# Kernel tuning notes

Hardware: AMD Instinct MI355X
Metric: run time of the kernel (lower is better)

## Reference

```python
import jax, jax.numpy as jnp
import numpy as np
from jax import lax

B, L = 16, 2048
D_TOK, D_TIS = 256, 64
D_MODEL = D_TOK + D_TIS          # 320
EXPAND = 2
D_INNER = EXPAND * D_MODEL       # 640
D_STATE = 16
D_CONV = 4
DT_RANK = (D_MODEL + 15) // 16   # 20 (ceil(d_model/16), Mamba default)
H_OUT = 128
VOCAB = 65                       # len(CODON_MAP_DNA)+1
N_TISSUES = 30
MAX_NORM = 2.0


def _embed_maxnorm(W, idx):
    # torch nn.Embedding(max_norm=2): looked-up rows are renormalized to norm<=2
    e = W[idx]
    n = jnp.linalg.norm(e, axis=-1, keepdims=True)
    return e * jnp.minimum(1.0, MAX_NORM / jnp.maximum(n, 1e-12))


def setup_inputs() -> dict:
    key = jax.random.key(0)
    ks = jax.random.split(key, 18)
    s = 0.02
    seq_W = jax.random.normal(ks[3], (VOCAB, D_TOK), dtype=jnp.float32)
    seq_W = seq_W.at[0].set(0.0)  # padding_idx=0
    A_log = jnp.log(jnp.broadcast_to(jnp.arange(1, D_STATE + 1, dtype=jnp.float32), (D_INNER, D_STATE)))
    return {
        "rna_data_pad": jax.random.randint(ks[0], (B, L), 0, VOCAB).astype(jnp.int32),
        "tissue_id": jax.random.randint(ks[1], (B,), 0, N_TISSUES).astype(jnp.int32),
        "seq_lengths": jax.random.randint(ks[2], (B,), 1, L + 1).astype(jnp.int32),
        "seq_W": seq_W,
        "tissue_W": jax.random.normal(ks[4], (N_TISSUES, D_TIS), dtype=jnp.float32),
        "in_proj_W": jax.random.normal(ks[5], (2 * D_INNER, D_MODEL), dtype=jnp.float32) * s,
        "conv_w": jax.random.normal(ks[6], (D_INNER, 1, D_CONV), dtype=jnp.float32) * s,
        "conv_b": jnp.zeros((D_INNER,), dtype=jnp.float32),
        "x_proj_W": jax.random.normal(ks[7], (DT_RANK + 2 * D_STATE, D_INNER), dtype=jnp.float32) * s,
        "dt_proj_W": jax.random.normal(ks[8], (D_INNER, DT_RANK), dtype=jnp.float32) * s,
        "dt_proj_b": jax.random.uniform(ks[9], (D_INNER,), minval=-4.0, maxval=-2.0),
        "A_log": A_log,
        "D_skip": jnp.ones((D_INNER,), dtype=jnp.float32),
        "out_proj_W": jax.random.normal(ks[10], (D_MODEL, D_INNER), dtype=jnp.float32) * s,
        "p1_W": jax.random.normal(ks[11], (H_OUT, D_MODEL), dtype=jnp.float32) * s,
        "p1_b": jnp.zeros((H_OUT,), dtype=jnp.float32),
        "p2_W": jax.random.normal(ks[12], (1, H_OUT), dtype=jnp.float32) * s,
        "p2_b": jnp.zeros((1,), dtype=jnp.float32),
    }


def reference(rna_data_pad, tissue_id, seq_lengths, seq_W, tissue_W, in_proj_W,
              conv_w, conv_b, x_proj_W, dt_proj_W, dt_proj_b, A_log, D_skip,
              out_proj_W, p1_W, p1_b, p2_W, p2_b):
    b, l = rna_data_pad.shape
    # embeddings + tissue broadcast + mask
    seq_emb = _embed_maxnorm(seq_W, rna_data_pad)            # [B,L,D_TOK]
    tis_emb = _embed_maxnorm(tissue_W, tissue_id)            # [B,D_TIS]
    tis_exp = jnp.broadcast_to(tis_emb[:, None, :], (b, l, tis_emb.shape[-1]))
    x = jnp.concatenate([seq_emb, tis_exp], axis=-1)          # [B,L,D_MODEL]
    x = x * (rna_data_pad != 0)[..., None]
    # Mamba block
    xz = x @ in_proj_W.T                                      # [B,L,2*D_INNER]
    xm, z = jnp.split(xz, 2, axis=-1)
    xt = xm.transpose(0, 2, 1)                                # [B,D_INNER,L]
    conv = lax.conv_general_dilated(
        xt, conv_w, window_strides=(1,), padding=[(D_CONV - 1, 0)],
        feature_group_count=D_INNER,
        dimension_numbers=("NCH", "OIH", "NCH")) + conv_b[None, :, None]
    xm = jax.nn.silu(conv).transpose(0, 2, 1)                 # [B,L,D_INNER]
    x_dbl = xm @ x_proj_W.T                                   # [B,L,DT_RANK+2*D_STATE]
    dt, Bm, Cm = jnp.split(x_dbl, [DT_RANK, DT_RANK + D_STATE], axis=-1)
    delta = jax.nn.softplus(dt @ dt_proj_W.T + dt_proj_b)     # [B,L,D_INNER]
    A = -jnp.exp(A_log)                                       # [D_INNER,D_STATE]
    # selective scan over time
    xs = (delta.transpose(1, 0, 2), Bm.transpose(1, 0, 2),
          Cm.transpose(1, 0, 2), xm.transpose(1, 0, 2))
    h0 = jnp.zeros((b, D_INNER, D_STATE), dtype=xm.dtype)

    def step(h, t):
        dl, bt, ct, ut = t                                    # [B,di],[B,ds],[B,ds],[B,di]
        dA = jnp.exp(dl[:, :, None] * A)                      # [B,di,ds]
        dBu = (dl * ut)[:, :, None] * bt[:, None, :]          # [B,di,ds]
        h = dA * h + dBu
        y = jnp.einsum("bds,bs->bd", h, ct)
        return h, y

    _, ys = lax.scan(step, h0, xs)                            # ys: [L,B,D_INNER]
    y = ys.transpose(1, 0, 2) + xm * D_skip
    y = y * jax.nn.silu(z)
    out = y @ out_proj_W.T                                    # [B,L,D_MODEL]
    # gather last valid timestep
    out_last = out[jnp.arange(b), seq_lengths - 1]            # [B,D_MODEL]
    h1 = jax.nn.relu(out_last @ p1_W.T + p1_b)
    return h1 @ p2_W.T + p2_b                                 # [B,1]
```

## Files before the change

### kernel.cpp

```cpp
#include <hip/hip_runtime.h>
#include <hip/hip_bf16.h>
#include <math.h>

#define B_      16
#define L_      2048
#define D_MODEL 320
#define D_INNER 640
#define D_STATE 16
#define DT_RANK 20
#define H_OUT   128
#define VOCAB   65
#define N_TIS   30
#define TT      8
#define ST      64
#define NCHUNK  16
#define CHLEN   (L_/NCHUNK)

static constexpr size_t OFF_MSEQ  = 0;
static constexpr size_t OFF_MTIS  = OFF_MSEQ + VOCAB*1280;
static constexpr size_t OFF_YSCAN = OFF_MTIS + N_TIS*1280;
static constexpr size_t OFF_CLAST = OFF_YSCAN + B_*D_INNER;
static constexpr size_t OFF_XD20  = OFF_CLAST + B_*16;
static constexpr size_t OFF_BBAR  = OFF_XD20 + (size_t)B_*L_*20;
static constexpr size_t OFF_PC    = OFF_BBAR + (size_t)B_*D_STATE*L_;
static constexpr size_t OFF_SC    = OFF_PC + (size_t)B_*NCHUNK*40*256;

__device__ __forceinline__ float silu_f(float x) { return x / (1.0f + __expf(-x)); }

__global__ __launch_bounds__(256) void k_mbuild(
    const float* __restrict__ seqW, const float* __restrict__ tisW,
    const float* __restrict__ inW, float* __restrict__ ws)
{
    __shared__ float a_l[256];
    __shared__ float red[4];
    int v = blockIdx.x, tid = threadIdx.x;
    int K, wofs; const float* src; float* dstM;
    if (v < VOCAB) { K = 256; wofs = 0;   src = seqW + (size_t)v*256;        dstM = ws + OFF_MSEQ + (size_t)v*1280; }
    else           { K = 64;  wofs = 256; src = tisW + (size_t)(v-VOCAB)*64; dstM = ws + OFF_MTIS + (size_t)(v-VOCAB)*1280; }
    float x = (tid < K) ? src[tid] : 0.0f;
    float ss = x * x;
    #pragma unroll
    for (int o = 32; o; o >>= 1) ss += __shfl_xor(ss, o);
    if ((tid & 63) == 0) red[tid >> 6] = ss;
    __syncthreads();
    float tot = red[0] + red[1] + red[2] + red[3];
    float scale = fminf(1.0f, 2.0f / fmaxf(sqrtf(tot), 1e-12f));
    if (tid < K) a_l[tid] = x * scale;
    __syncthreads();

    int j = blockIdx.y * 256 + tid;
    const float* w = inW + (size_t)j*320 + wofs;
    float ac0 = 0.f, ac1 = 0.f, ac2 = 0.f, ac3 = 0.f;
    #pragma unroll 4
    for (int k = 0; k < K; k += 4) {
        float4 w4 = *(const float4*)(w + k);
        ac0 += a_l[k+0]*w4.x; ac1 += a_l[k+1]*w4.y;
        ac2 += a_l[k+2]*w4.z; ac3 += a_l[k+3]*w4.w;
    }
    dstM[j] = (ac0 + ac1) + (ac2 + ac3);
}

__global__ __launch_bounds__(256) void k_xdbl(
    const int* __restrict__ idx, const int* __restrict__ tissue_id,
    const int* __restrict__ seq_lengths,
    const float* __restrict__ conv_w, const float* __restrict__ conv_b,
    const float* __restrict__ xW, float* __restrict__ ws)
{
    __shared__ float u_l[TT*641];
    __shared__ float xd_l[TT*36];
    __shared__ int   idx_l[TT+3];
    int b = blockIdx.y;
    int t0 = blockIdx.x * TT;
    int t_last = seq_lengths[b] - 1;
    if (t0 > t_last) return;
    int tid = threadIdx.x;
    const float* Mseq = ws + OFF_MSEQ;
    const float* Mtis = ws + OFF_MTIS;
    int tis = tissue_id[b];
    if (tid < TT+3) {
        int t = t0 - 3 + tid;
        idx_l[tid] = (t >= 0) ? idx[b*L_ + t] : 0;
    }
    __syncthreads();

    for (int d = tid; d < D_INNER; d += 256) {
        float w0 = conv_w[d*4+0], w1 = conv_w[d*4+1], w2 = conv_w[d*4+2], w3 = conv_w[d*4+3];
        float cb = conv_b[d];
        float mt = Mtis[(size_t)tis*1280 + d];
        float xzv[TT+3];
        #pragma unroll
        for (int k = 0; k < TT+3; ++k) {
            int row = idx_l[k];
            xzv[k] = row ? (Mseq[(size_t)row*1280 + d] + mt) : 0.0f;
        }
        #pragma unroll
        for (int t = 0; t < TT; ++t) {
            float c = cb;
            c = fmaf(w0, xzv[t+0], c);
            c = fmaf(w1, xzv[t+1], c);
            c = fmaf(w2, xzv[t+2], c);
            c = fmaf(w3, xzv[t+3], c);
            u_l[t*641 + d] = silu_f(c);
        }
    }
    __syncthreads();

    {
        int w = tid >> 6, l = tid & 63;
        float wreg[9][10];
        #pragma unroll
        for (int kk = 0; kk < 9; ++kk) {
            const float* xr = xW + (size_t)(w + 4*kk)*D_INNER + l;
            #pragma unroll
            for (int i = 0; i < 10; ++i) wreg[kk][i] = xr[64*i];
        }
        for (int t = 0; t < TT; ++t) {
            float p[9];
            #pragma unroll
            for (int kk = 0; kk < 9; ++kk) p[kk] = 0.f;
            #pragma unroll
            for (int i = 0; i < 10; ++i) {
                float ui = u_l[t*641 + l + 64*i];
                #pragma unroll
                for (int kk = 0; kk < 9; ++kk) p[kk] = fmaf(wreg[kk][i], ui, p[kk]);
            }
            #pragma unroll
            for (int o = 32; o; o >>= 1) {
                #pragma unroll
                for (int kk = 0; kk < 9; ++kk) p[kk] += __shfl_xor(p[kk], o);
            }
            if (l == t) {
                #pragma unroll
                for (int kk = 0; kk < 9; ++kk) xd_l[t*36 + w + 4*kk] = p[kk];
            }
        }
        if (t_last < t0 + TT) {
            int tl = t_last - t0;
            float pc[4];
            #pragma unroll
            for (int k = 0; k < 4; ++k) pc[k] = 0.f;
            #pragma unroll
            for (int i = 0; i < 10; ++i) {
                float ui = u_l[tl*641 + l + 64*i];
                #pragma unroll
                for (int k = 0; k < 4; ++k)
                    pc[k] = fmaf(xW[(size_t)(36 + w + 4*k)*D_INNER + l + 64*i], ui, pc[k]);
            }
            #pragma unroll
            for (int o = 32; o; o >>= 1) {
                #pragma unroll
                for (int k = 0; k < 4; ++k) pc[k] += __shfl_xor(pc[k], o);
            }
            if (l == 0) {
                #pragma unroll
                for (int k = 0; k < 4; ++k) ws[OFF_CLAST + b*16 + w + 4*k] = pc[k];
            }
        }
    }
    __syncthreads();

    {
        int nt = min(TT, t_last - t0 + 1);
        int cnt = nt * 20;
        float* dst = ws + OFF_XD20 + ((size_t)b*L_ + t0)*20;
        for (int o = tid; o < cnt; o += 256) {
            int t = o / 20, r = o - t*20;
            dst[o] = xd_l[t*36 + r];
        }
        int cntB = nt * 16;
        if (tid < cntB) {
            int s, tt;
            if (nt == TT) { s = tid >> 3; tt = tid & 7; }
            else          { s = tid / nt; tt = tid - s*nt; }
            ws[OFF_BBAR + ((size_t)b*D_STATE + s)*L_ + t0 + tt] = xd_l[tt*36 + 20 + s];
        }
    }
}

__global__ __launch_bounds__(256) void k_scanc(
    const int* __restrict__ idx, const int* __restrict__ tissue_id,
    const int* __restrict__ seq_lengths,
    const float* __restrict__ conv_w, const float* __restrict__ conv_b,
    const float* __restrict__ dtW, const float* __restrict__ dtb,
    const float* __restrict__ A_log, float* __restrict__ ws)
{
    __shared__ float xd_t[ST*20];
    __shared__ float dl_t[16*68];
    __shared__ float du_t[16*68];
    __shared__ float Bb_t[16*68];
    __shared__ float sdred[16*17];
    __shared__ int   idx_t[ST+3];

    int b = blockIdx.y, dg = blockIdx.x, c = blockIdx.z;
    int t_last = seq_lengths[b] - 1;
    int t_begin = c * CHLEN;
    if (t_begin > t_last) return;
    int t_end = min(t_begin + CHLEN - 1, t_last);
    int tid = threadIdx.x;
    int dl = tid >> 4, s = tid & 15;
    int dd = tid & 15, tg = tid >> 4;
    int d_own = dg*16 + dd;
    int tis = tissue_id[b];
    const float* Mseq = ws + OFF_MSEQ;

    float dtw_r[20];
    #pragma unroll
    for (int i = 0; i < 20; i += 4) {
        float4 w4 = *(const float4*)(dtW + d_own*20 + i);
        dtw_r[i] = w4.x; dtw_r[i+1] = w4.y; dtw_r[i+2] = w4.z; dtw_r[i+3] = w4.w;
    }
    float4 cw4 = *(const float4*)(conv_w + d_own*4);
    float  cb  = conv_b[d_own];
    float  dtb_v = dtb[d_own];
    float  mt  = ws[OFF_MTIS + (size_t)tis*1280 + d_own];
    float As = -__expf(A_log[(dg*16 + dl)*D_STATE + s]) * 1.44269504089f;

    float h = 0.0f;
    float sdp = 0.0f;
    for (int t0 = t_begin; t0 <= t_end; t0 += ST) {
        int nt = min(ST, t_end - t0 + 1);
        if (tid < ST+3) {
            int t = t0 - 3 + tid;
            idx_t[tid] = (t >= 0 && t < L_) ? idx[b*L_ + t] : 0;
        }
        {
            const float4* src = (const float4*)(ws + OFF_XD20 + ((size_t)b*L_ + t0)*20);
            float4* dst = (float4*)xd_t;
            int cnt4 = nt * 5;
            for (int o = tid; o < cnt4; o += 256) dst[o] = src[o];
        }
        {
            int lr = tid >> 4, c4 = (tid & 15) * 4;
            if (c4 < nt)
                *(float4*)(Bb_t + lr*68 + c4) =
                    *(const float4*)(ws + OFF_BBAR + ((size_t)b*D_STATE + lr)*L_ + t0 + c4);
        }
        __syncthreads();

        {
            int ttb = tg * 4;
            if (ttb < nt) {
                float xz[7];
                #pragma unroll
                for (int k = 0; k < 7; ++k) {
                    int row = idx_t[ttb + k];
                    xz[k] = row ? (Mseq[(size_t)row*1280 + d_own] + mt) : 0.0f;
                }
                float dl4[4], du4[4];
                bool full = (ttb + 3 < nt);
                #pragma unroll
                for (int j = 0; j < 4; ++j) {
                    int tt = ttb + j;
                    if (full || tt < nt) {
                        float cc = cb;
                        cc = fmaf(cw4.x, xz[j+0], cc);
                        cc = fmaf(cw4.y, xz[j+1], cc);
                        cc = fmaf(cw4.z, xz[j+2], cc);
                        cc = fmaf(cw4.w, xz[j+3], cc);
                        float u = silu_f(cc);
                        const float* xr = xd_t + tt*20;
                        float x = dtb_v;
                        #pragma unroll
                        for (int r = 0; r < 20; r += 4) {
                            float4 x4 = *(const float4*)(xr + r);
                            x = fmaf(x4.x, dtw_r[r+0], x);
                            x = fmaf(x4.y, dtw_r[r+1], x);
                            x = fmaf(x4.z, dtw_r[r+2], x);
                            x = fmaf(x4.w, dtw_r[r+3], x);
                        }
                        float e = __expf(-fabsf(x));
                        float sp = fmaxf(x, 0.0f) + __logf(1.0f + e);
                        dl4[j] = sp;
                        du4[j] = sp * u;
                        sdp += sp;
                    } else { dl4[j] = 0.f; du4[j] = 0.f; }
                }
                if (full) {
                    *(float4*)(dl_t + dd*68 + ttb) = make_float4(dl4[0], dl4[1], dl4[2], dl4[3]);
                    *(float4*)(du_t + dd*68 + ttb) = make_float4(du4[0], du4[1], du4[2], du4[3]);
                } else {
                    for (int j = 0; j < 4 && ttb + j < nt; ++j) {
                        dl_t[dd*68 + ttb + j] = dl4[j];
                        du_t[dd*68 + ttb + j] = du4[j];
                    }
                }
            }
        }
        __syncthreads();

        {
            int q4 = nt >> 2;
            #pragma unroll 8
            for (int q = 0; q < q4; ++q) {
                float4 d4 = *(const float4*)(dl_t + dl*68 + 4*q);
                float4 u4 = *(const float4*)(du_t + dl*68 + 4*q);
                float4 b4 = *(const float4*)(Bb_t + s*68 + 4*q);
                h = fmaf(exp2f(d4.x*As), h, u4.x*b4.x);
                h = fmaf(exp2f(d4.y*As), h, u4.y*b4.y);
                h = fmaf(exp2f(d4.z*As), h, u4.z*b4.z);
                h = fmaf(exp2f(d4.w*As), h, u4.w*b4.w);
            }
            for (int tt = q4*4; tt < nt; ++tt) {
                float dlt = dl_t[dl*68 + tt];
                h = fmaf(exp2f(dlt * As), h, du_t[dl*68 + tt] * Bb_t[s*68 + tt]);
            }
        }
        __syncthreads();
    }
    sdred[tg*17 + dd] = sdp;
    __syncthreads();
    float sd = 0.0f;
    #pragma unroll
    for (int g = 0; g < 16; ++g) sd += sdred[g*17 + dl];
    float P = exp2f(As * sd);
    size_t base = (((size_t)b*NCHUNK + c)*40 + dg)*256 + tid;
    ws[OFF_PC + base] = P;
    ws[OFF_SC + base] = h;
}

__global__ __launch_bounds__(256) void k_comb(const int* __restrict__ seq_lengths,
                                              float* __restrict__ ws)
{
    int b = blockIdx.y, dg = blockIdx.x;
    int tid = threadIdx.x;
    int dl = tid >> 4, s = tid & 15;
    int t_last = seq_lengths[b] - 1;
    int ncv = t_last / CHLEN + 1;
    float h = 0.0f;
    for (int c = 0; c < ncv; ++c) {
        size_t base = (((size_t)b*NCHUNK + c)*40 + dg)*256 + tid;
        h = fmaf(ws[OFF_PC + base], h, ws[OFF_SC + base]);
    }
    float v = h * ws[OFF_CLAST + b*16 + s];
    v += __shfl_xor(v, 1); v += __shfl_xor(v, 2);
    v += __shfl_xor(v, 4); v += __shfl_xor(v, 8);
    if (s == 0) ws[OFF_YSCAN + (size_t)b*D_INNER + dg*16 + dl] = v;
}

__global__ __launch_bounds__(320) void k_final(
    const int* __restrict__ idx, const int* __restrict__ tissue_id,
    const int* __restrict__ seq_lengths,
    const float* __restrict__ conv_w, const float* __restrict__ conv_b,
    const float* __restrict__ Dskip, const float* __restrict__ outW,
    const float* __restrict__ p1W, const float* __restrict__ p1b,
    const float* __restrict__ p2W, const float* __restrict__ p2b,
    const float* __restrict__ ws, float* __restrict__ out)
{
    __shared__ float y_l[D_INNER];
    __shared__ float o_l[D_MODEL];
    __shared__ float h1_l[H_OUT];
    int b = blockIdx.x, tid = threadIdx.x;
    int t_last = seq_lengths[b] - 1;
    int tis = tissue_id[b];
    const float* Mseq = ws + OFF_MSEQ;
    const float* Mtis = ws + OFF_MTIS;
    int rows[4];
    #pragma unroll
    for (int k = 0; k < 4; ++k) {
        int t = t_last - 3 + k;
        rows[k] = (t >= 0) ? idx[b*L_ + t] : 0;
    }
    for (int d = tid; d < D_INNER; d += 320) {
        float conv = conv_b[d];
        const float* cw = conv_w + d*4;
        #pragma unroll
        for (int k = 0; k < 4; ++k) {
            int row = rows[k];
            float xzv = row ? (Mseq[(size_t)row*1280 + d] + Mtis[(size_t)tis*1280 + d]) : 0.0f;
            conv += cw[k] * xzv;
        }
        float u = silu_f(conv);
        int rowL = rows[3];
        float z = rowL ? (Mseq[(size_t)rowL*1280 + 640 + d] + Mtis[(size_t)tis*1280 + 640 + d]) : 0.0f;
        float ys = ws[OFF_YSCAN + (size_t)b*D_INNER + d];
        y_l[d] = (ys + u * Dskip[d]) * silu_f(z);
    }
    __syncthreads();
    if (tid < D_MODEL) {
        const float* w = outW + tid*D_INNER;
        float acc = 0.f;
        #pragma unroll 4
        for (int k = 0; k < D_INNER; k += 4) {
            float4 w4 = *(const float4*)(w + k);
            acc += y_l[k]*w4.x + y_l[k+1]*w4.y + y_l[k+2]*w4.z + y_l[k+3]*w4.w;
        }
        o_l[tid] = acc;
    }
    __syncthreads();
    if (tid < H_OUT) {
        const float* w = p1W + tid*D_MODEL;
        float acc = p1b[tid];
        #pragma unroll 4
        for (int k = 0; k < D_MODEL; k += 4) {
            float4 w4 = *(const float4*)(w + k);
            acc += o_l[k]*w4.x + o_l[k+1]*w4.y + o_l[k+2]*w4.z + o_l[k+3]*w4.w;
        }
        h1_l[tid] = fmaxf(acc, 0.0f);
    }
    __syncthreads();
    if (tid == 0) {
        float acc = p2b[0];
        for (int k = 0; k < H_OUT; ++k) acc += h1_l[k]*p2W[k];
        out[b] = acc;
    }
}

extern "C" void kernel_launch(void* const* d_in, const int* in_sizes, int n_in,
                              void* d_out, int out_size, void* d_ws, size_t ws_size,
                              hipStream_t stream)
{
    const int*   idx   = (const int*)d_in[0];
    const int*   tis   = (const int*)d_in[1];
    const int*   slen  = (const int*)d_in[2];
    const float* seqW  = (const float*)d_in[3];
    const float* tisW  = (const float*)d_in[4];
    const float* inW   = (const float*)d_in[5];
    const float* convw = (const float*)d_in[6];
    const float* convb = (const float*)d_in[7];
    const float* xW    = (const float*)d_in[8];
    const float* dtW   = (const float*)d_in[9];
    const float* dtb   = (const float*)d_in[10];
    const float* Alog  = (const float*)d_in[11];
    const float* Dsk   = (const float*)d_in[12];
    const float* outW  = (const float*)d_in[13];
    const float* p1W   = (const float*)d_in[14];
    const float* p1b   = (const float*)d_in[15];
    const float* p2W   = (const float*)d_in[16];
    const float* p2b   = (const float*)d_in[17];
    float* ws  = (float*)d_ws;
    float* out = (float*)d_out;

    hipLaunchKernelGGL(k_mbuild, dim3(VOCAB + N_TIS, 5), dim3(256), 0, stream, seqW, tisW, inW, ws);
    hipLaunchKernelGGL(k_xdbl,   dim3(L_/TT, B_),        dim3(256), 0, stream,
                       idx, tis, slen, convw, convb, xW, ws);
    hipLaunchKernelGGL(k_scanc,  dim3(D_INNER/16, B_, NCHUNK), dim3(256), 0, stream,
                       idx, tis, slen, convw, convb, dtW, dtb, Alog, ws);
    hipLaunchKernelGGL(k_comb,   dim3(D_INNER/16, B_),   dim3(256), 0, stream, slen, ws);
    hipLaunchKernelGGL(k_final,  dim3(B_),               dim3(320), 0, stream,
                       idx, tis, slen, convw, convb, Dsk, outW, p1W, p1b, p2W, p2b, ws, out);
}
```

Before: 273.2 us.

## Micro-optimize kernels: transpose-reduce shuffles, fast rcp silu, unsigned indexing, grid remap

Several unrelated micro-optimizations. k_mbuild now has each wavefront compute 64 output rows with coalesced float4 weight reads and a butterfly reduction, instead of one thread striding a whole row. k_xdbl's 9-way wave reduction becomes a transpose-style shuffle tree that needs fewer shuffles. SiLU uses a hardware reciprocal, gather offsets use 32-bit unsigned arithmetic, and the k_scanc grid is flattened so chunks of the same channel group are adjacent in launch order. Exp and product computations in the scan loop are hoisted off the dependency chain. The approximate reciprocal adds small numerical error.

```diff
diff --git a/kernel.cpp b/kernel.cpp
--- a/kernel.cpp
+++ b/kernel.cpp
@@ -25,7 +25,8 @@
 static constexpr size_t OFF_PC    = OFF_BBAR + (size_t)B_*D_STATE*L_;
 static constexpr size_t OFF_SC    = OFF_PC + (size_t)B_*NCHUNK*40*256;
 
-__device__ __forceinline__ float silu_f(float x) { return x / (1.0f + __expf(-x)); }
+__device__ __forceinline__ float fast_rcp(float x) { return __builtin_amdgcn_rcpf(x); }
+__device__ __forceinline__ float silu_f(float x) { return x * fast_rcp(1.0f + __expf(-x)); }
 
 __global__ __launch_bounds__(256) void k_mbuild(
     const float* __restrict__ seqW, const float* __restrict__ tisW,
@@ -45,19 +46,32 @@
     __syncthreads();
     float tot = red[0] + red[1] + red[2] + red[3];
     float scale = fminf(1.0f, 2.0f / fmaxf(sqrtf(tot), 1e-12f));
-    if (tid < K) a_l[tid] = x * scale;
-    __syncthreads();
-
-    int j = blockIdx.y * 256 + tid;
-    const float* w = inW + (size_t)j*320 + wofs;
-    float ac0 = 0.f, ac1 = 0.f, ac2 = 0.f, ac3 = 0.f;
-    #pragma unroll 4
-    for (int k = 0; k < K; k += 4) {
-        float4 w4 = *(const float4*)(w + k);
-        ac0 += a_l[k+0]*w4.x; ac1 += a_l[k+1]*w4.y;
-        ac2 += a_l[k+2]*w4.z; ac3 += a_l[k+3]*w4.w;
-    }
-    dstM[j] = (ac0 + ac1) + (ac2 + ac3);
+    a_l[tid] = (tid < K) ? x * scale : 0.0f;
+    __syncthreads();
+
+    int wv = tid >> 6, l = tid & 63;
+    float4 a4 = ((const float4*)a_l)[l];
+    int j0 = blockIdx.y * 256 + wv * 64;
+    bool lane_on = (4*l < K);
+    for (int jj = 0; jj < 64; jj += 4) {
+        float p[4];
+        #pragma unroll
+        for (int u = 0; u < 4; ++u) {
+            float pv = 0.0f;
+            if (lane_on) {
+                const float4 w4 = *(const float4*)(inW + (size_t)(j0 + jj + u)*320 + wofs + 4*l);
+                pv = a4.x*w4.x + a4.y*w4.y + a4.z*w4.z + a4.w*w4.w;
+            }
+            p[u] = pv;
+        }
+        float ta, tb;
+        ta=__shfl_xor(p[0],1); tb=__shfl_xor(p[1],1); p[0]=(l&1)?(p[1]+tb):(p[0]+ta);
+        ta=__shfl_xor(p[2],1); tb=__shfl_xor(p[3],1); p[2]=(l&1)?(p[3]+tb):(p[2]+ta);
+        ta=__shfl_xor(p[0],2); tb=__shfl_xor(p[2],2); p[0]=(l&2)?(p[2]+tb):(p[0]+ta);
+        p[0]+=__shfl_xor(p[0],4);  p[0]+=__shfl_xor(p[0],8);
+        p[0]+=__shfl_xor(p[0],16); p[0]+=__shfl_xor(p[0],32);
+        if (l < 4) dstM[j0 + jj + l] = p[0];
+    }
 }
 
 __global__ __launch_bounds__(256) void k_xdbl(
@@ -90,8 +104,8 @@
         float xzv[TT+3];
         #pragma unroll
         for (int k = 0; k < TT+3; ++k) {
-            int row = idx_l[k];
-            xzv[k] = row ? (Mseq[(size_t)row*1280 + d] + mt) : 0.0f;
+            unsigned ro = (unsigned)idx_l[k] * 1280u;
+            xzv[k] = ro ? (Mseq[ro + (unsigned)d] + mt) : 0.0f;
         }
         #pragma unroll
         for (int t = 0; t < TT; ++t) {
@@ -124,15 +138,23 @@
                 #pragma unroll
                 for (int kk = 0; kk < 9; ++kk) p[kk] = fmaf(wreg[kk][i], ui, p[kk]);
             }
-            #pragma unroll
-            for (int o = 32; o; o >>= 1) {
-                #pragma unroll
-                for (int kk = 0; kk < 9; ++kk) p[kk] += __shfl_xor(p[kk], o);
-            }
-            if (l == t) {
-                #pragma unroll
-                for (int kk = 0; kk < 9; ++kk) xd_l[t*36 + w + 4*kk] = p[kk];
-            }
+            {
+                float ta, tb;
+                ta=__shfl_xor(p[0],1); tb=__shfl_xor(p[1],1); p[0]=(l&1)?(p[1]+tb):(p[0]+ta);
+                ta=__shfl_xor(p[2],1); tb=__shfl_xor(p[3],1); p[2]=(l&1)?(p[3]+tb):(p[2]+ta);
+                ta=__shfl_xor(p[4],1); tb=__shfl_xor(p[5],1); p[4]=(l&1)?(p[5]+tb):(p[4]+ta);
+                ta=__shfl_xor(p[6],1); tb=__shfl_xor(p[7],1); p[6]=(l&1)?(p[7]+tb):(p[6]+ta);
+                p[8]+=__shfl_xor(p[8],1);
+                ta=__shfl_xor(p[0],2); tb=__shfl_xor(p[2],2); p[0]=(l&2)?(p[2]+tb):(p[0]+ta);
+                ta=__shfl_xor(p[4],2); tb=__shfl_xor(p[6],2); p[4]=(l&2)?(p[6]+tb):(p[4]+ta);
+                p[8]+=__shfl_xor(p[8],2);
+                ta=__shfl_xor(p[0],4); tb=__shfl_xor(p[4],4); p[0]=(l&4)?(p[4]+tb):(p[0]+ta);
+                p[8]+=__shfl_xor(p[8],4);
+                ta=__shfl_xor(p[0],8); tb=__shfl_xor(p[8],8); p[0]=(l&8)?(p[8]+tb):(p[0]+ta);
+                p[0]+=__shfl_xor(p[0],16);
+                p[0]+=__shfl_xor(p[0],32);
+            }
+            if (l < 9) xd_l[t*36 + w + 4*l] = p[0];
         }
         if (t_last < t0 + TT) {
             int tl = t_last - t0;
@@ -191,7 +213,10 @@
     __shared__ float sdred[16*17];
     __shared__ int   idx_t[ST+3];
 
-    int b = blockIdx.y, dg = blockIdx.x, c = blockIdx.z;
+    int bx = blockIdx.x;
+    int c  = bx & (NCHUNK-1);
+    int dg = bx >> 4;
+    int b  = blockIdx.y;
     int t_last = seq_lengths[b] - 1;
     int t_begin = c * CHLEN;
     if (t_begin > t_last) return;
@@ -200,6 +225,7 @@
     int dl = tid >> 4, s = tid & 15;
     int dd = tid & 15, tg = tid >> 4;
     int d_own = dg*16 + dd;
+    unsigned dco = (unsigned)d_own;
     int tis = tissue_id[b];
     const float* Mseq = ws + OFF_MSEQ;
 
@@ -243,8 +269,8 @@
                 float xz[7];
                 #pragma unroll
                 for (int k = 0; k < 7; ++k) {
-                    int row = idx_t[ttb + k];
-                    xz[k] = row ? (Mseq[(size_t)row*1280 + d_own] + mt) : 0.0f;
+                    unsigned ro = (unsigned)idx_t[ttb + k] * 1280u;
+                    xz[k] = ro ? (Mseq[ro + dco] + mt) : 0.0f;
                 }
                 float dl4[4], du4[4];
                 bool full = (ttb + 3 < nt);
@@ -295,10 +321,12 @@
                 float4 d4 = *(const float4*)(dl_t + dl*68 + 4*q);
                 float4 u4 = *(const float4*)(du_t + dl*68 + 4*q);
                 float4 b4 = *(const float4*)(Bb_t + s*68 + 4*q);
-                h = fmaf(exp2f(d4.x*As), h, u4.x*b4.x);
-                h = fmaf(exp2f(d4.y*As), h, u4.y*b4.y);
-                h = fmaf(exp2f(d4.z*As), h, u4.z*b4.z);
-                h = fmaf(exp2f(d4.w*As), h, u4.w*b4.w);
+                float e0 = exp2f(d4.x*As), e1 = exp2f(d4.y*As);
+                float e2 = exp2f(d4.z*As), e3 = exp2f(d4.w*As);
+                float c0 = u4.x*b4.x, c1 = u4.y*b4.y;
+                float c2 = u4.z*b4.z, c3 = u4.w*b4.w;
+                h = fmaf(e0, h, c0); h = fmaf(e1, h, c1);
+                h = fmaf(e2, h, c2); h = fmaf(e3, h, c3);
             }
             for (int tt = q4*4; tt < nt; ++tt) {
                 float dlt = dl_t[dl*68 + tt];
@@ -365,13 +393,13 @@
         const float* cw = conv_w + d*4;
         #pragma unroll
         for (int k = 0; k < 4; ++k) {
-            int row = rows[k];
-            float xzv = row ? (Mseq[(size_t)row*1280 + d] + Mtis[(size_t)tis*1280 + d]) : 0.0f;
+            unsigned ro = (unsigned)rows[k] * 1280u;
+            float xzv = ro ? (Mseq[ro + (unsigned)d] + Mtis[(size_t)tis*1280 + d]) : 0.0f;
             conv += cw[k] * xzv;
         }
         float u = silu_f(conv);
-        int rowL = rows[3];
-        float z = rowL ? (Mseq[(size_t)rowL*1280 + 640 + d] + Mtis[(size_t)tis*1280 + 640 + d]) : 0.0f;
+        unsigned roL = (unsigned)rows[3] * 1280u;
+        float z = roL ? (Mseq[roL + 640u + (unsigned)d] + Mtis[(size_t)tis*1280 + 640 + d]) : 0.0f;
         float ys = ws[OFF_YSCAN + (size_t)b*D_INNER + d];
         y_l[d] = (ys + u * Dskip[d]) * silu_f(z);
     }
@@ -433,7 +461,7 @@
     hipLaunchKernelGGL(k_mbuild, dim3(VOCAB + N_TIS, 5), dim3(256), 0, stream, seqW, tisW, inW, ws);
     hipLaunchKernelGGL(k_xdbl,   dim3(L_/TT, B_),        dim3(256), 0, stream,
                        idx, tis, slen, convw, convb, xW, ws);
-    hipLaunchKernelGGL(k_scanc,  dim3(D_INNER/16, B_, NCHUNK), dim3(256), 0, stream,
+    hipLaunchKernelGGL(k_scanc,  dim3(NCHUNK * (D_INNER/16), B_), dim3(256), 0, stream,
                        idx, tis, slen, convw, convb, dtW, dtb, Alog, ws);
     hipLaunchKernelGGL(k_comb,   dim3(D_INNER/16, B_),   dim3(256), 0, stream, slen, ws);
     hipLaunchKernelGGL(k_final,  dim3(B_),               dim3(320), 0, stream,
```

Result: slower. 309.0 us (+13.1%).
